# Kernel tuning notes

Measured on AMD Instinct MI355X. Metric: run time of the kernel, lower is better.

Reference implementation:

```python
import jax, jax.numpy as jnp
import numpy as np


def setup_inputs() -> dict:
    key = jax.random.key(0)
    k1, k2, k3 = jax.random.split(key, 3)
    B, T, D = 2, 2048, 1024
    x = jax.random.normal(k1, (B, T, D), dtype=jnp.float32)
    w_qkv = jax.random.normal(k2, (3 * D, D), dtype=jnp.float32) * (D ** -0.5)
    w_out = jax.random.normal(k3, (D, D), dtype=jnp.float32) * (D ** -0.5)
    return {"x": x, "w_qkv": w_qkv, "w_out": w_out, "heads": 16}


def reference(x, w_qkv, w_out, heads):
    # SelfAttention forward: attention_type='sdp', position_mode='alibi', causal=True, eval mode.
    B, T, D = x.shape
    H = heads
    hd = D // H
    scale = hd ** -0.5

    # qkv projection: torch Linear -> x @ W^T
    qkv = (x @ w_qkv.T).reshape(B, T, 3, H, hd)
    qkv = jnp.transpose(qkv, (2, 0, 3, 1, 4))  # [3, B, H, T, hd]
    q, k, v = qkv[0], qkv[1], qkv[2]

    # ALiBi relative bias: slopes = 1 / 2^(h/H) for h = 1..H
    slopes = 1.0 / jnp.power(2.0, jnp.arange(1, H + 1, dtype=jnp.float32) / H)
    pos = jnp.arange(T, dtype=jnp.float32)
    rel = jnp.abs(pos[:, None] - pos[None, :])  # [T, T]
    bias = -slopes[None, :, None, None] * rel[None, None, :, :]  # [1, H, T, T]

    # scores + causal mask + softmax (manual path since position_bias is not None)
    scores = jnp.einsum('bhqd,bhkd->bhqk', q, k) * scale + bias
    causal_mask = jnp.triu(jnp.ones((T, T), dtype=bool), k=1)
    scores = jnp.where(causal_mask[None, None, :, :], -jnp.inf, scores)
    attn = jax.nn.softmax(scores, axis=-1)
    attn = jnp.where(jnp.isnan(attn), 1.0 / float(max(T, 1)), attn)

    out = jnp.einsum('bhqk,bhkd->bhqd', attn, v)  # [B, H, T, hd]
    out = jnp.transpose(out, (0, 2, 1, 3)).reshape(B, T, D)
    return out @ w_out.T
```

## Files before the change

### kernel.cpp

```cpp
#include <hip/hip_runtime.h>
#include <hip/hip_bf16.h>

typedef __attribute__((ext_vector_type(8))) short shortx8;
typedef __attribute__((ext_vector_type(4))) float floatx4;
typedef __attribute__((ext_vector_type(16))) float floatx16;
typedef __attribute__((ext_vector_type(4))) unsigned uintx4;
typedef __attribute__((ext_vector_type(2))) unsigned uintx2;

#define B_ 2
#define T_ 2048
#define D_ 1024
#define H_ 16
#define HD_ 64
#define SCALE 0.125f
#define QSCALE 0.18033688011112042f
#define SMAX2 23.083120654223414f
#define FULLH ((size_t)B_ * H_ * T_ * HD_)

#define GLDS16(g, l) __builtin_amdgcn_global_load_lds( \
    (__attribute__((address_space(1))) void*)(g), \
    (__attribute__((address_space(3))) void*)(l), 16, 0, 0)

__device__ __forceinline__ short f2bf(float f) {
    union { float f; unsigned u; } v; v.f = f;
    unsigned r = v.u + 0x7FFFu + ((v.u >> 16) & 1u);
    return (short)(r >> 16);
}

__device__ __forceinline__ unsigned pk2(float x, float y) {
    union { __hip_bfloat162 h; unsigned u; } t;
    t.h = __float22bfloat162_rn(make_float2(x, y));
    return t.u;
}

__device__ __forceinline__ shortx8 cvt8(floatx4 a, floatx4 b) {
    uintx4 r = { pk2(a[0], a[1]), pk2(a[2], a[3]), pk2(b[0], b[1]), pk2(b[2], b[3]) };
    return __builtin_bit_cast(shortx8, r);
}

__device__ __forceinline__ float ex2(float x) {
#if __has_builtin(__builtin_amdgcn_exp2f)
    return __builtin_amdgcn_exp2f(x);
#else
    return exp2f(x);
#endif
}

__global__ __launch_bounds__(256) void cvt_xw(const float* __restrict__ x,
                                              const float* __restrict__ wqkv,
                                              short* __restrict__ xbf,
                                              short* __restrict__ wbf) {
    int i = blockIdx.x * 256 + threadIdx.x;
    const float* src; short* dst; int o;
    if (i < 524288) { src = x; dst = xbf; o = i; }
    else            { src = wqkv; dst = wbf; o = i - 524288; }
    const floatx4* p = reinterpret_cast<const floatx4*>(src) + (size_t)o * 2;
    *(reinterpret_cast<shortx8*>(dst) + o) = cvt8(p[0], p[1]);
}

__global__ __launch_bounds__(256) void qkv_fast(const short* __restrict__ xbf,
                                                const short* __restrict__ wbf,
                                                short* __restrict__ qout,
                                                short* __restrict__ kv) {
    __shared__ __align__(16) short As[128 * 64];
    __shared__ __align__(16) short Bs[128 * 64];

    const int tid = threadIdx.x;
    const int wv = tid >> 6;
    const int l  = tid & 63;
    const int ln = l & 15;
    const int quad = l >> 4;
    const int rowb = quad << 2;
    const int wm = wv >> 1, wn = wv & 1;
    const int m0 = blockIdx.y * 128;
    const int n0g = blockIdx.x * 128;

    const int lr = l >> 3, lc = l & 7;
    const int gcol = (lc ^ lr) << 3;
    const short* agp = xbf + (size_t)(m0 + wv * 32 + lr) * D_ + gcol;
    const short* bgp = wbf + (size_t)(n0g + wv * 32 + lr) * D_ + gcol;
    short* aldsb = As + wv * 32 * 64;
    short* bldsb = Bs + wv * 32 * 64;

    floatx4 acc[4][4] = {};

    for (int k0 = 0; k0 < D_; k0 += 64) {
        __syncthreads();
#pragma unroll
        for (int c = 0; c < 4; ++c) {
            GLDS16(agp + (size_t)(c * 8) * D_ + k0, aldsb + c * 512);
            GLDS16(bgp + (size_t)(c * 8) * D_ + k0, bldsb + c * 512);
        }
        __syncthreads();

#pragma unroll
        for (int kk = 0; kk < 2; ++kk) {
            const int csw = (kk << 2) + quad;
            const int sw = (csw ^ (ln & 7)) << 3;
            shortx8 af[4], bf[4];
#pragma unroll
            for (int i = 0; i < 4; ++i)
                af[i] = *reinterpret_cast<const shortx8*>(&As[((wm * 64 + i * 16 + ln) << 6) + sw]);
#pragma unroll
            for (int j = 0; j < 4; ++j)
                bf[j] = *reinterpret_cast<const shortx8*>(&Bs[((wn * 64 + j * 16 + ln) << 6) + sw]);
#pragma unroll
            for (int i = 0; i < 4; ++i)
#pragma unroll
                for (int j = 0; j < 4; ++j)
                    acc[i][j] = __builtin_amdgcn_mfma_f32_16x16x32_bf16(af[i], bf[j], acc[i][j], 0, 0, 0);
        }
    }

    const int sel = n0g >> 10;
    const int bb = m0 >> 11;
    const int t0w = (m0 + wm * 64) & (T_ - 1);
    const int h = ((n0g + wn * 64) >> 6) & 15;

    if (sel < 2) {
        short* dst = (sel == 0) ? qout : kv;
        const float sc = (sel == 0) ? QSCALE : 1.0f;
        const size_t hb = (size_t)(bb * H_ + h) * T_;
#pragma unroll
        for (int i = 0; i < 4; ++i)
#pragma unroll
            for (int r = 0; r < 4; ++r) {
                int t = t0w + i * 16 + rowb + r;
#pragma unroll
                for (int j = 0; j < 4; ++j)
                    dst[(hb + t) * HD_ + j * 16 + ln] = f2bf(acc[i][j][r] * sc);
            }
    } else {
        __syncthreads();
        short* tb = (wv < 2) ? (As + wv * 4096) : (Bs + (wv - 2) * 4096);
        short* vhead = kv + FULLH + (size_t)(bb * H_ + h) * HD_ * T_;
        const int dl = l & 31, th = (l >> 5) << 5;
#pragma unroll
        for (int p = 0; p < 2; ++p) {
#pragma unroll
            for (int i = 0; i < 4; ++i)
#pragma unroll
                for (int jj = 0; jj < 2; ++jj) {
                    int j = 2 * p + jj;
#pragma unroll
                    for (int r = 0; r < 4; ++r)
                        tb[(jj * 16 + ln) * 72 + i * 16 + rowb + r] = f2bf(acc[i][j][r]);
                }
            short* vd = vhead + (size_t)(p * 32 + dl) * T_ + t0w + th;
#pragma unroll
            for (int seg = 0; seg < 4; ++seg)
                *reinterpret_cast<shortx8*>(vd + seg * 8) =
                    *reinterpret_cast<const shortx8*>(&tb[dl * 72 + th + seg * 8]);
        }
    }
}

__global__ __launch_bounds__(256) void out_fast(const short* __restrict__ Abf,
                                                const short* __restrict__ wbf,
                                                float* __restrict__ out) {
    __shared__ __align__(16) short As[128 * 64];
    __shared__ __align__(16) short Bs[128 * 64];

    const int tid = threadIdx.x;
    const int wv = tid >> 6;
    const int l  = tid & 63;
    const int ln = l & 15;
    const int quad = l >> 4;
    const int rowb = quad << 2;
    const int wm = wv >> 1, wn = wv & 1;
    const int m0 = blockIdx.y * 128;
    const int n0g = blockIdx.x * 128;

    const int lr = l >> 3, lc = l & 7;
    const int gcol = (lc ^ lr) << 3;
    const short* bgp = wbf + (size_t)(n0g + wv * 32 + lr) * D_ + gcol;
    short* aldsb = As + wv * 32 * 64;
    short* bldsb = Bs + wv * 32 * 64;

    size_t abase[4];
#pragma unroll
    for (int c = 0; c < 4; ++c) {
        int m = m0 + wv * 32 + c * 8 + lr;
        int bb2 = m >> 11, t = m & (T_ - 1);
        abase[c] = ((size_t)(bb2 * H_) * T_ + t) * HD_ + gcol;
    }

    floatx4 acc[4][4] = {};

    for (int k0 = 0; k0 < D_; k0 += 64) {
        const size_t hoff = (size_t)(k0 >> 6) * T_ * HD_;
        __syncthreads();
#pragma unroll
        for (int c = 0; c < 4; ++c) {
            GLDS16(Abf + abase[c] + hoff, aldsb + c * 512);
            GLDS16(bgp + (size_t)(c * 8) * D_ + k0, bldsb + c * 512);
        }
        __syncthreads();

#pragma unroll
        for (int kk = 0; kk < 2; ++kk) {
            const int csw = (kk << 2) + quad;
            const int sw = (csw ^ (ln & 7)) << 3;
            shortx8 af[4], bf[4];
#pragma unroll
            for (int i = 0; i < 4; ++i)
                af[i] = *reinterpret_cast<const shortx8*>(&As[((wm * 64 + i * 16 + ln) << 6) + sw]);
#pragma unroll
            for (int j = 0; j < 4; ++j)
                bf[j] = *reinterpret_cast<const shortx8*>(&Bs[((wn * 64 + j * 16 + ln) << 6) + sw]);
#pragma unroll
            for (int i = 0; i < 4; ++i)
#pragma unroll
                for (int j = 0; j < 4; ++j)
                    acc[i][j] = __builtin_amdgcn_mfma_f32_16x16x32_bf16(af[i], bf[j], acc[i][j], 0, 0, 0);
        }
    }

#pragma unroll
    for (int i = 0; i < 4; ++i)
#pragma unroll
        for (int r = 0; r < 4; ++r) {
            int m = m0 + wm * 64 + i * 16 + rowb + r;
#pragma unroll
            for (int j = 0; j < 4; ++j)
                out[(size_t)m * D_ + n0g + wn * 64 + j * 16 + ln] = acc[i][j][r];
        }
}

__device__ __forceinline__ void attn_group(int g, int ql, int hi, float slope2,
                                           size_t koff,
                                           const short* __restrict__ qws,
                                           const short* __restrict__ kbase,
                                           const short* __restrict__ vbase,
                                           short* __restrict__ ao) {
    const int q0w = g * 32;
    const int e = (g >> 1) + 1;
    const int parity = g & 1;
    const int qlh = ql - 4 * hi;
    const float s32 = slope2 * 32.0f;

    shortx8 qf[4];
#pragma unroll
    for (int ds = 0; ds < 4; ++ds)
        qf[ds] = *reinterpret_cast<const shortx8*>(&qws[koff + (size_t)(q0w + ql) * HD_ + ds * 16 + hi * 8]);

    const float cbase = slope2 * (float)(4 * hi - (q0w + ql)) - SMAX2;
    float rb[16];
#pragma unroll
    for (int t = 0; t < 16; ++t)
        rb[t] = cbase + slope2 * (float)((t & 3) + 8 * (t >> 2));

    floatx16 o0 = {}, o1 = {}, ls = {};
    const shortx8 ones = {16256, 16256, 16256, 16256, 16256, 16256, 16256, 16256};

    const short* kq  = kbase + ql * HD_ + hi * 8;
    const short* vq0 = vbase + (size_t)ql * T_ + hi * 8;
    const short* vq1 = vbase + (size_t)(32 + ql) * T_ + hi * 8;

    shortx8 kA[2][4], kB[2][4], vf[2][4];

    auto LK = [&](int kb, shortx8 (&dst)[2][4]) {
#pragma unroll
        for (int nc = 0; nc < 2; ++nc)
#pragma unroll
            for (int ds = 0; ds < 4; ++ds)
                dst[nc][ds] = *reinterpret_cast<const shortx8*>(kq + (kb * 64 + nc * 32) * HD_ + ds * 16);
    };
    auto LV = [&](int kb) {
#pragma unroll
        for (int ks = 0; ks < 4; ++ks) {
            vf[0][ks] = *reinterpret_cast<const shortx8*>(vq0 + kb * 64 + ks * 16);
            vf[1][ks] = *reinterpret_cast<const shortx8*>(vq1 + kb * 64 + ks * 16);
        }
    };
    auto COMP = [&](const shortx8 (&kc)[2][4], int kb) {
        const bool last = (kb == e - 1);
        const float tb = slope2 * (float)(kb * 64);
#pragma unroll
        for (int nc = 0; nc < 2; ++nc) {
            if (last && nc > parity) continue;
            const bool part = last && (nc == parity);
            floatx16 s = {};
#pragma unroll
            for (int ds = 0; ds < 4; ++ds)
                s = __builtin_amdgcn_mfma_f32_32x32x16_bf16(kc[nc][ds], qf[ds], s, 0, 0, 0);
            const float tnc = tb + (nc ? s32 : 0.0f);
            float p[16];
#pragma unroll
            for (int t = 0; t < 16; ++t) {
                float ev = ex2(s[t] + (rb[t] + tnc));
                if (part) {
                    const int kc2 = (t & 3) + 8 * (t >> 2);
                    ev = (kc2 <= qlh) ? ev : 0.0f;
                }
                p[t] = ev;
            }
            unsigned cv[4][2];
#pragma unroll
            for (int t = 0; t < 4; ++t) {
                cv[t][0] = pk2(p[4 * t + 0], p[4 * t + 1]);
                cv[t][1] = pk2(p[4 * t + 2], p[4 * t + 3]);
            }
            __builtin_amdgcn_s_setprio(1);
#pragma unroll
            for (int kh = 0; kh < 2; ++kh) {
                unsigned w0 = cv[2 * kh][0], w2 = cv[2 * kh + 1][0];
                unsigned w1 = cv[2 * kh][1], w3 = cv[2 * kh + 1][1];
                asm volatile("v_permlane32_swap_b32 %0, %1" : "+v"(w0), "+v"(w2));
                asm volatile("v_permlane32_swap_b32 %0, %1" : "+v"(w1), "+v"(w3));
                uintx4 uu = {w0, w1, w2, w3};
                shortx8 apv = __builtin_bit_cast(shortx8, uu);
                const int ks = nc * 2 + kh;
                ls = __builtin_amdgcn_mfma_f32_32x32x16_bf16(apv, ones, ls, 0, 0, 0);
                o0 = __builtin_amdgcn_mfma_f32_32x32x16_bf16(apv, vf[0][ks], o0, 0, 0, 0);
                o1 = __builtin_amdgcn_mfma_f32_32x32x16_bf16(apv, vf[1][ks], o1, 0, 0, 0);
            }
            __builtin_amdgcn_s_setprio(0);
        }
    };

    LK(0, kA);
    int kb = 0;
    for (;;) {
        LV(kb);
        if (kb + 1 < e) LK(kb + 1, kB);
        COMP(kA, kb);
        ++kb; if (kb == e) break;
        LV(kb);
        if (kb + 1 < e) LK(kb + 1, kA);
        COMP(kB, kb);
        ++kb; if (kb == e) break;
    }

#pragma unroll
    for (int t = 0; t < 16; ++t) {
        const int qrow = (t & 3) + 8 * (t >> 2) + 4 * hi;
        const float inv = 1.0f / ls[t];
        const size_t ob = koff + (size_t)(q0w + qrow) * HD_ + ql;
        ao[ob]      = f2bf(o0[t] * inv);
        ao[ob + 32] = f2bf(o1[t] * inv);
    }
}

__global__ __launch_bounds__(64, 1) void attn(const short* __restrict__ qws,
                                              const short* __restrict__ kv,
                                              short* ao,
                                              const float* __restrict__ wout,
                                              short* __restrict__ wobf) {
    if (blockIdx.x >= 1024) {
        int i = (blockIdx.x - 1024) * 64 + threadIdx.x;
        const floatx4* p = reinterpret_cast<const floatx4*>(wout) + (size_t)i * 2;
        *(reinterpret_cast<shortx8*>(wobf) + i) = cvt8(p[0], p[1]);
        return;
    }
    const int l  = threadIdx.x;
    const int ql = l & 31, hi = l >> 5;
    const int id  = blockIdx.x;
    const int xcd = id & 7;
    const int u2  = (id >> 3) & 3;
    const int pr  = id >> 5;
    const int bh  = xcd * 4 + u2;
    const int h = bh & 15, b = bh >> 4;

    const float slope2 = 1.4426950408889634f * exp2f(-(float)(h + 1) * 0.0625f);
    const size_t koff = (size_t)(b * H_ + h) * T_ * HD_;
    const short* kbase = kv + koff;
    const short* vbase = kv + FULLH + koff;

    attn_group(63 - pr, ql, hi, slope2, koff, qws, kbase, vbase, ao);
    attn_group(pr,      ql, hi, slope2, koff, qws, kbase, vbase, ao);
}

__global__ __launch_bounds__(256) void qkv_slow(const float* __restrict__ x,
                                                const float* __restrict__ wqkv,
                                                short* __restrict__ qout,
                                                short* __restrict__ kv) {
    __shared__ __align__(16) short As[64][72];
    __shared__ __align__(16) short Bs[64][72];
    const int tid = threadIdx.x;
    const int wv = tid >> 6, l = tid & 63, ln = l & 15, quad = l >> 4, qd = quad << 3;
    const int m0 = blockIdx.y * 64;
    const int sel = blockIdx.x >> 4, h = blockIdx.x & 15;
    const int nrow = sel * D_ + h * HD_;
    const int sr0 = tid >> 3, sc0 = (tid & 7) << 3, sr1 = sr0 + 32;
    floatx4 fa[4], fb[4];
    auto FETCH = [&](int k0) {
        const float* ap = &x[(size_t)(m0 + sr0) * D_ + k0 + sc0];
        fa[0] = *reinterpret_cast<const floatx4*>(ap);
        fa[1] = *reinterpret_cast<const floatx4*>(ap + 4);
        ap += (size_t)32 * D_;
        fa[2] = *reinterpret_cast<const floatx4*>(ap);
        fa[3] = *reinterpret_cast<const floatx4*>(ap + 4);
        const float* bp = &wqkv[(size_t)(nrow + sr0) * D_ + k0 + sc0];
        fb[0] = *reinterpret_cast<const floatx4*>(bp);
        fb[1] = *reinterpret_cast<const floatx4*>(bp + 4);
        bp += (size_t)32 * D_;
        fb[2] = *reinterpret_cast<const floatx4*>(bp);
        fb[3] = *reinterpret_cast<const floatx4*>(bp + 4);
    };
    floatx4 acc[4] = {};
    FETCH(0);
    for (int k0 = 0; k0 < D_; k0 += 64) {
        __syncthreads();
        *reinterpret_cast<shortx8*>(&As[sr0][sc0]) = cvt8(fa[0], fa[1]);
        *reinterpret_cast<shortx8*>(&As[sr1][sc0]) = cvt8(fa[2], fa[3]);
        *reinterpret_cast<shortx8*>(&Bs[sr0][sc0]) = cvt8(fb[0], fb[1]);
        *reinterpret_cast<shortx8*>(&Bs[sr1][sc0]) = cvt8(fb[2], fb[3]);
        __syncthreads();
        if (k0 + 64 < D_) FETCH(k0 + 64);
        const int mr = (wv << 4) + ln;
#pragma unroll
        for (int kk = 0; kk < 2; ++kk) {
            shortx8 a = *reinterpret_cast<const shortx8*>(&As[mr][kk * 32 + qd]);
#pragma unroll
            for (int nc = 0; nc < 4; ++nc) {
                shortx8 bq = *reinterpret_cast<const shortx8*>(&Bs[nc * 16 + ln][kk * 32 + qd]);
                acc[nc] = __builtin_amdgcn_mfma_f32_16x16x32_bf16(a, bq, acc[nc], 0, 0, 0);
            }
        }
    }
    const int bb = m0 >> 11, t0 = m0 & (T_ - 1);
    if (sel < 2) {
        short* dst = (sel == 0) ? qout : kv;
        const float sc = (sel == 0) ? QSCALE : 1.0f;
#pragma unroll
        for (int r = 0; r < 4; ++r) {
            int t = t0 + (wv << 4) + (quad << 2) + r;
#pragma unroll
            for (int nc = 0; nc < 4; ++nc)
                dst[((size_t)(bb * H_ + h) * T_ + t) * HD_ + nc * 16 + ln] = f2bf(acc[nc][r] * sc);
        }
    } else {
        __syncthreads();
#pragma unroll
        for (int r = 0; r < 4; ++r)
#pragma unroll
            for (int nc = 0; nc < 4; ++nc)
                As[nc * 16 + ln][(wv << 4) + (quad << 2) + r] = f2bf(acc[nc][r]);
        __syncthreads();
        const int d = tid >> 2, tseg = (tid & 3) << 4;
        short* vdst = kv + FULLH + ((size_t)(bb * H_ + h) * HD_ + d) * T_ + t0 + tseg;
        *reinterpret_cast<shortx8*>(vdst)     = *reinterpret_cast<const shortx8*>(&As[d][tseg]);
        *reinterpret_cast<shortx8*>(vdst + 8) = *reinterpret_cast<const shortx8*>(&As[d][tseg + 8]);
    }
}

__global__ __launch_bounds__(256) void out_slow(const short* __restrict__ A,
                                                const float* __restrict__ W,
                                                float* __restrict__ out) {
    __shared__ __align__(16) short As[64][72];
    __shared__ __align__(16) short Bs[64][72];
    const int tid = threadIdx.x;
    const int wv = tid >> 6, l = tid & 63, ln = l & 15, quad = l >> 4, qd = quad << 3;
    const int m0 = blockIdx.y * 64, n0 = blockIdx.x * 64;
    const int sr0 = tid >> 3, sc0 = (tid & 7) << 3, sr1 = sr0 + 32;
    shortx8 sa0, sa1;
    floatx4 fb[4];
    auto FETCH = [&](int k0) {
        const int h = k0 >> 6;
        int m = m0 + sr0;
        int bb = m >> 11, t = m & (T_ - 1);
        sa0 = *reinterpret_cast<const shortx8*>(A + ((size_t)(bb * H_ + h) * T_ + t) * HD_ + sc0);
        m = m0 + sr1; bb = m >> 11; t = m & (T_ - 1);
        sa1 = *reinterpret_cast<const shortx8*>(A + ((size_t)(bb * H_ + h) * T_ + t) * HD_ + sc0);
        const float* bp = &W[(size_t)(n0 + sr0) * D_ + k0 + sc0];
        fb[0] = *reinterpret_cast<const floatx4*>(bp);
        fb[1] = *reinterpret_cast<const floatx4*>(bp + 4);
        bp += (size_t)32 * D_;
        fb[2] = *reinterpret_cast<const floatx4*>(bp);
        fb[3] = *reinterpret_cast<const floatx4*>(bp + 4);
    };
    floatx4 acc[4] = {};
    FETCH(0);
    for (int k0 = 0; k0 < D_; k0 += 64) {
        __syncthreads();
        *reinterpret_cast<shortx8*>(&As[sr0][sc0]) = sa0;
        *reinterpret_cast<shortx8*>(&As[sr1][sc0]) = sa1;
        *reinterpret_cast<shortx8*>(&Bs[sr0][sc0]) = cvt8(fb[0], fb[1]);
        *reinterpret_cast<shortx8*>(&Bs[sr1][sc0]) = cvt8(fb[2], fb[3]);
        __syncthreads();
        if (k0 + 64 < D_) FETCH(k0 + 64);
        const int mr = (wv << 4) + ln;
#pragma unroll
        for (int kk = 0; kk < 2; ++kk) {
            shortx8 a = *reinterpret_cast<const shortx8*>(&As[mr][kk * 32 + qd]);
#pragma unroll
            for (int nc = 0; nc < 4; ++nc) {
                shortx8 bq = *reinterpret_cast<const shortx8*>(&Bs[nc * 16 + ln][kk * 32 + qd]);
                acc[nc] = __builtin_amdgcn_mfma_f32_16x16x32_bf16(a, bq, acc[nc], 0, 0, 0);
            }
        }
    }
#pragma unroll
    for (int r = 0; r < 4; ++r) {
        int m = m0 + (wv << 4) + (quad << 2) + r;
#pragma unroll
        for (int nc = 0; nc < 4; ++nc)
            out[(size_t)m * D_ + n0 + nc * 16 + ln] = acc[nc][r];
    }
}

extern "C" void kernel_launch(void* const* d_in, const int* in_sizes, int n_in,
                              void* d_out, int out_size, void* d_ws, size_t ws_size,
                              hipStream_t stream) {
    const float* x    = (const float*)d_in[0];
    const float* wqkv = (const float*)d_in[1];
    const float* wout = (const float*)d_in[2];

    short* kvbuf = (short*)d_out;
    float* out   = (float*)d_out;

    if (ws_size >= 23068672ULL) {
        short* xbf  = (short*)d_ws;
        short* wbf  = xbf + 4 * 1024 * 1024;
        short* qws  = xbf + 7 * 1024 * 1024;
        short* wobf = xbf;

        cvt_xw<<<3584, 256, 0, stream>>>(x, wqkv, xbf, wbf);
        qkv_fast<<<dim3(24, 32), 256, 0, stream>>>(xbf, wbf, qws, kvbuf);
        attn<<<dim3(3072), 64, 0, stream>>>(qws, kvbuf, qws, wout, wobf);
        out_fast<<<dim3(8, 32), 256, 0, stream>>>(qws, wobf, out);
    } else {
        short* qws = (short*)d_ws;
        qkv_slow<<<dim3(48, 64), 256, 0, stream>>>(x, wqkv, qws, kvbuf);
        attn<<<dim3(1024), 64, 0, stream>>>(qws, kvbuf, qws, nullptr, nullptr);
        out_slow<<<dim3(16, 64), 256, 0, stream>>>(qws, wout, out);
    }
}
```

Measured before the change: 206.0 us.

## Give each attention workgroup one query group and double-buffer V loads

The attention kernel previously paired a long and a short causal query group inside one 64-thread block. It now launches one block per query group, interleaving long and short groups by block index, and raises launch bounds to two blocks per CU. V fragments are also double-buffered and prefetched alongside K, one step ahead. This adds parallelism and occupancy, at the cost of more registers per wave and a less deterministic causal load balance.

```diff
diff --git a/kernel.cpp b/kernel.cpp
--- a/kernel.cpp
+++ b/kernel.cpp
@@ -227,12 +227,32 @@
         }
 }
 
-__device__ __forceinline__ void attn_group(int g, int ql, int hi, float slope2,
-                                           size_t koff,
-                                           const short* __restrict__ qws,
-                                           const short* __restrict__ kbase,
-                                           const short* __restrict__ vbase,
-                                           short* __restrict__ ao) {
+__global__ __launch_bounds__(64, 2) void attn(const short* __restrict__ qws,
+                                              const short* __restrict__ kv,
+                                              short* ao,
+                                              const float* __restrict__ wout,
+                                              short* __restrict__ wobf) {
+    if (blockIdx.x >= 2048) {
+        int i = (blockIdx.x - 2048) * 64 + threadIdx.x;
+        const floatx4* p = reinterpret_cast<const floatx4*>(wout) + (size_t)i * 2;
+        *(reinterpret_cast<shortx8*>(wobf) + i) = cvt8(p[0], p[1]);
+        return;
+    }
+    const int l  = threadIdx.x;
+    const int ql = l & 31, hi = l >> 5;
+    const int id  = blockIdx.x;
+    const int xcd = id & 7;
+    const int u2  = (id >> 3) & 3;
+    const int s   = id >> 5;
+    const int g   = (s & 1) ? (s >> 1) : 63 - (s >> 1);
+    const int bh  = xcd * 4 + u2;
+    const int h = bh & 15, b = bh >> 4;
+
+    const float slope2 = 1.4426950408889634f * exp2f(-(float)(h + 1) * 0.0625f);
+    const size_t koff = (size_t)(b * H_ + h) * T_ * HD_;
+    const short* kbase = kv + koff;
+    const short* vbase = kv + FULLH + koff;
+
     const int q0w = g * 32;
     const int e = (g >> 1) + 1;
     const int parity = g & 1;
@@ -257,7 +277,7 @@
     const short* vq0 = vbase + (size_t)ql * T_ + hi * 8;
     const short* vq1 = vbase + (size_t)(32 + ql) * T_ + hi * 8;
 
-    shortx8 kA[2][4], kB[2][4], vf[2][4];
+    shortx8 kA[2][4], kB[2][4], vA[2][4], vB[2][4];
 
     auto LK = [&](int kb, shortx8 (&dst)[2][4]) {
 #pragma unroll
@@ -266,29 +286,29 @@
             for (int ds = 0; ds < 4; ++ds)
                 dst[nc][ds] = *reinterpret_cast<const shortx8*>(kq + (kb * 64 + nc * 32) * HD_ + ds * 16);
     };
-    auto LV = [&](int kb) {
+    auto LV = [&](int kb, shortx8 (&dst)[2][4]) {
 #pragma unroll
         for (int ks = 0; ks < 4; ++ks) {
-            vf[0][ks] = *reinterpret_cast<const shortx8*>(vq0 + kb * 64 + ks * 16);
-            vf[1][ks] = *reinterpret_cast<const shortx8*>(vq1 + kb * 64 + ks * 16);
+            dst[0][ks] = *reinterpret_cast<const shortx8*>(vq0 + kb * 64 + ks * 16);
+            dst[1][ks] = *reinterpret_cast<const shortx8*>(vq1 + kb * 64 + ks * 16);
         }
     };
-    auto COMP = [&](const shortx8 (&kc)[2][4], int kb) {
+    auto COMP = [&](const shortx8 (&kc)[2][4], const shortx8 (&vf)[2][4], int kb) {
         const bool last = (kb == e - 1);
         const float tb = slope2 * (float)(kb * 64);
 #pragma unroll
         for (int nc = 0; nc < 2; ++nc) {
             if (last && nc > parity) continue;
             const bool part = last && (nc == parity);
-            floatx16 s = {};
+            floatx16 sacc = {};
 #pragma unroll
             for (int ds = 0; ds < 4; ++ds)
-                s = __builtin_amdgcn_mfma_f32_32x32x16_bf16(kc[nc][ds], qf[ds], s, 0, 0, 0);
+                sacc = __builtin_amdgcn_mfma_f32_32x32x16_bf16(kc[nc][ds], qf[ds], sacc, 0, 0, 0);
             const float tnc = tb + (nc ? s32 : 0.0f);
             float p[16];
 #pragma unroll
             for (int t = 0; t < 16; ++t) {
-                float ev = ex2(s[t] + (rb[t] + tnc));
+                float ev = ex2(sacc[t] + (rb[t] + tnc));
                 if (part) {
                     const int kc2 = (t & 3) + 8 * (t >> 2);
                     ev = (kc2 <= qlh) ? ev : 0.0f;
@@ -319,16 +339,14 @@
         }
     };
 
-    LK(0, kA);
+    LK(0, kA); LV(0, vA);
     int kb = 0;
     for (;;) {
-        LV(kb);
-        if (kb + 1 < e) LK(kb + 1, kB);
-        COMP(kA, kb);
+        if (kb + 1 < e) { LK(kb + 1, kB); LV(kb + 1, vB); }
+        COMP(kA, vA, kb);
         ++kb; if (kb == e) break;
-        LV(kb);
-        if (kb + 1 < e) LK(kb + 1, kA);
-        COMP(kB, kb);
+        if (kb + 1 < e) { LK(kb + 1, kA); LV(kb + 1, vA); }
+        COMP(kB, vB, kb);
         ++kb; if (kb == e) break;
     }
 
@@ -340,35 +358,6 @@
         ao[ob]      = f2bf(o0[t] * inv);
         ao[ob + 32] = f2bf(o1[t] * inv);
     }
-}
-
-__global__ __launch_bounds__(64, 1) void attn(const short* __restrict__ qws,
-                                              const short* __restrict__ kv,
-                                              short* ao,
-                                              const float* __restrict__ wout,
-                                              short* __restrict__ wobf) {
-    if (blockIdx.x >= 1024) {
-        int i = (blockIdx.x - 1024) * 64 + threadIdx.x;
-        const floatx4* p = reinterpret_cast<const floatx4*>(wout) + (size_t)i * 2;
-        *(reinterpret_cast<shortx8*>(wobf) + i) = cvt8(p[0], p[1]);
-        return;
-    }
-    const int l  = threadIdx.x;
-    const int ql = l & 31, hi = l >> 5;
-    const int id  = blockIdx.x;
-    const int xcd = id & 7;
-    const int u2  = (id >> 3) & 3;
-    const int pr  = id >> 5;
-    const int bh  = xcd * 4 + u2;
-    const int h = bh & 15, b = bh >> 4;
-
-    const float slope2 = 1.4426950408889634f * exp2f(-(float)(h + 1) * 0.0625f);
-    const size_t koff = (size_t)(b * H_ + h) * T_ * HD_;
-    const short* kbase = kv + koff;
-    const short* vbase = kv + FULLH + koff;
-
-    attn_group(63 - pr, ql, hi, slope2, koff, qws, kbase, vbase, ao);
-    attn_group(pr,      ql, hi, slope2, koff, qws, kbase, vbase, ao);
 }
 
 __global__ __launch_bounds__(256) void qkv_slow(const float* __restrict__ x,
@@ -518,12 +507,12 @@
 
         cvt_xw<<<3584, 256, 0, stream>>>(x, wqkv, xbf, wbf);
         qkv_fast<<<dim3(24, 32), 256, 0, stream>>>(xbf, wbf, qws, kvbuf);
-        attn<<<dim3(3072), 64, 0, stream>>>(qws, kvbuf, qws, wout, wobf);
+        attn<<<dim3(4096), 64, 0, stream>>>(qws, kvbuf, qws, wout, wobf);
         out_fast<<<dim3(8, 32), 256, 0, stream>>>(qws, wobf, out);
     } else {
         short* qws = (short*)d_ws;
         qkv_slow<<<dim3(48, 64), 256, 0, stream>>>(x, wqkv, qws, kvbuf);
-        attn<<<dim3(1024), 64, 0, stream>>>(qws, kvbuf, qws, nullptr, nullptr);
+        attn<<<dim3(2048), 64, 0, stream>>>(qws, kvbuf, qws, nullptr, nullptr);
         out_slow<<<dim3(16, 64), 256, 0, stream>>>(qws, wout, out);
     }
 }
```

Result: slower. 236.5 us (+14.8%).
